# Performance work log

Hardware: AMD Instinct MI355X
Metric: run time of the kernel (lower is better)

## Reference

```python
import jax, jax.numpy as jnp
import numpy as np

N_HEAD = 16
ROPE_THETA = 10000.0


def _rope_cache(T, dim, theta=ROPE_THETA):
    # inv_freq over even indices, as in RotaryEmbedding
    inv_freq = 1.0 / (theta ** (jnp.arange(0, dim, 2, dtype=jnp.float32) / dim))
    freqs = jnp.arange(T, dtype=jnp.float32)[:, None] * inv_freq[None, :]  # [T, dim//2]
    return jnp.cos(freqs), jnp.sin(freqs)


def _apply_rope(x, cos, sin):
    # x: [B, H, T, D]; cos/sin: [T, D//2] broadcast over B,H
    x1 = x[..., ::2]
    x2 = x[..., 1::2]
    # even slots: x1*cos - x2*sin ; odd slots: x2*cos + x1*sin (interleaved rotate-pairs)
    r1 = x1 * cos - x2 * sin
    r2 = x2 * cos + x1 * sin
    return jnp.stack([r1, r2], axis=-1).reshape(x.shape)


def setup_inputs() -> dict:
    key = jax.random.key(0)
    k1, k2, k3 = jax.random.split(key, 3)
    B, T, C = 4, 2048, 1024
    x = jax.random.normal(k1, (B, T, C), dtype=jnp.float32)
    W_qkv = jax.random.normal(k2, (C, 3 * C), dtype=jnp.float32) * (C ** -0.5)
    W_out = jax.random.normal(k3, (C, C), dtype=jnp.float32) * (C ** -0.5)
    return {"x": x, "W_qkv": W_qkv, "W_out": W_out}


def reference(x, W_qkv, W_out):
    B, T, C = x.shape
    H = N_HEAD
    D = C // H
    # fused QKV projection -> [3, B, H, T, D]
    qkv = (x @ W_qkv).reshape(B, T, 3, H, D).transpose(2, 0, 3, 1, 4)
    q, k, v = qkv[0], qkv[1], qkv[2]
    cos, sin = _rope_cache(T, D)
    q = _apply_rope(q, cos, sin)
    k = _apply_rope(k, cos, sin)
    scale = 1.0 / jnp.sqrt(jnp.float32(D))
    scores = jnp.einsum('bhqd,bhkd->bhqk', q, k) * scale  # [B,H,T,T]
    causal_mask = jnp.tril(jnp.ones((T, T), dtype=bool))
    scores = jnp.where(causal_mask, scores, -jnp.inf)
    attn = jax.nn.softmax(scores, axis=-1)
    out = jnp.einsum('bhqk,bhkd->bhqd', attn, v)  # [B,H,T,D]
    out = out.transpose(0, 2, 1, 3).reshape(B, T, C)
    return out @ W_out
```

## Files before the change

kernel.cpp:

```cpp
#include <hip/hip_runtime.h>
#include <math.h>

#define BATCH 4
#define SEQ   2048
#define CDIM  1024
#define NHEAD 16
#define HDIM  64
#define QKVN  3072
#define QSCALE 0.1803368801111244f

typedef float f32x4 __attribute__((ext_vector_type(4)));
typedef short bf16x8 __attribute__((ext_vector_type(8)));
typedef short bf16x4 __attribute__((ext_vector_type(4)));

static __device__ __forceinline__ unsigned short f2bf(float f) {
    unsigned int u = __float_as_uint(f);
    u += 0x7FFF + ((u >> 16) & 1);
    return (unsigned short)(u >> 16);
}
static __device__ __forceinline__ float bf2f(unsigned short u) {
    return __uint_as_float(((unsigned int)u) << 16);
}
static __device__ __forceinline__ bf16x8 lds_read8(const unsigned short* p) {
    bf16x4 lo = *(const bf16x4*)p;
    bf16x4 hi = *(const bf16x4*)(p + 4);
    return __builtin_shufflevector(lo, hi, 0, 1, 2, 3, 4, 5, 6, 7);
}

__global__ __launch_bounds__(256) void convert_bf16(const float* __restrict__ src,
                                                    unsigned short* __restrict__ dst,
                                                    int n4) {
    int i = blockIdx.x * 256 + threadIdx.x;
    if (i >= n4) return;
    float4 v = ((const float4*)src)[i];
    ushort4 o;
    o.x = f2bf(v.x); o.y = f2bf(v.y); o.z = f2bf(v.z); o.w = f2bf(v.w);
    ((ushort4*)dst)[i] = o;
}

__global__ __launch_bounds__(256) void transpose_bf16(const float* __restrict__ W,
                                                      unsigned short* __restrict__ Wt,
                                                      int K, int N) {
    __shared__ unsigned short tile[64][65];
    const int tid = threadIdx.x;
    const int n0 = blockIdx.x * 64;
    const int k0 = blockIdx.y * 64;
    const int r = tid >> 4;
    const int c4 = (tid & 15) << 2;
    #pragma unroll
    for (int ii = 0; ii < 4; ii++) {
        int row = r + 16 * ii;
        float4 v = *(const float4*)&W[(size_t)(k0 + row) * N + n0 + c4];
        tile[c4 + 0][row] = f2bf(v.x);
        tile[c4 + 1][row] = f2bf(v.y);
        tile[c4 + 2][row] = f2bf(v.z);
        tile[c4 + 3][row] = f2bf(v.w);
    }
    __syncthreads();
    #pragma unroll
    for (int ii = 0; ii < 4; ii++) {
        int row = r + 16 * ii;
        ushort4 o;
        o.x = tile[row][c4 + 0];
        o.y = tile[row][c4 + 1];
        o.z = tile[row][c4 + 2];
        o.w = tile[row][c4 + 3];
        *(ushort4*)&Wt[(size_t)(n0 + row) * K + k0 + c4] = o;
    }
}

#define GLDS(gp, lp) __builtin_amdgcn_global_load_lds(                       \
    (const __attribute__((address_space(1))) unsigned int*)(gp),             \
    (__attribute__((address_space(3))) unsigned int*)(lp), 16, 0, 0)

template <typename OUT>
__global__ __launch_bounds__(256) void gemm_bt_bf16(
    const unsigned short* __restrict__ A,
    const unsigned short* __restrict__ Bt,
    OUT* __restrict__ C, int M, int N, int K) {
    __shared__ unsigned short As[128 * 32];
    __shared__ unsigned short Bs[128 * 32];

    const int tid = threadIdx.x;
    const int wave = tid >> 6;
    const int lane = tid & 63;
    const int bm = blockIdx.y * 128;
    const int bn = blockIdx.x * 128;
    const int wm = (wave >> 1) * 64;
    const int wn = (wave & 1) * 64;

    const int srow = tid >> 2;
    const int scol = (tid & 3) << 3;
    const unsigned short* Ag0 = A + (size_t)(bm + srow) * K + scol;
    const unsigned short* Ag1 = A + (size_t)(bm + 64 + srow) * K + scol;
    const unsigned short* Bg0 = Bt + (size_t)(bn + srow) * K + scol;
    const unsigned short* Bg1 = Bt + (size_t)(bn + 64 + srow) * K + scol;
    char* AsW = (char*)As + wave * 1024;
    char* BsW = (char*)Bs + wave * 1024;

    const int fm = lane & 15;
    const int fq = (lane >> 4) << 3;

    f32x4 acc[4][4];
    #pragma unroll
    for (int i = 0; i < 4; i++)
        #pragma unroll
        for (int j = 0; j < 4; j++)
            acc[i][j] = (f32x4){0.f, 0.f, 0.f, 0.f};

    for (int k0 = 0; k0 < K; k0 += 32) {
        GLDS(Ag0 + k0, AsW);
        GLDS(Ag1 + k0, AsW + 4096);
        GLDS(Bg0 + k0, BsW);
        GLDS(Bg1 + k0, BsW + 4096);
        __syncthreads();

        bf16x8 af[4], bfr[4];
        #pragma unroll
        for (int i = 0; i < 4; i++)
            af[i] = *(const bf16x8*)&As[(wm + i * 16 + fm) * 32 + fq];
        #pragma unroll
        for (int j = 0; j < 4; j++)
            bfr[j] = *(const bf16x8*)&Bs[(wn + j * 16 + fm) * 32 + fq];
        #pragma unroll
        for (int i = 0; i < 4; i++)
            #pragma unroll
            for (int j = 0; j < 4; j++)
                acc[i][j] = __builtin_amdgcn_mfma_f32_16x16x32_bf16(
                    af[i], bfr[j], acc[i][j], 0, 0, 0);
        __syncthreads();
    }

    const int er = (lane >> 4) * 4;
    #pragma unroll
    for (int i = 0; i < 4; i++) {
        #pragma unroll
        for (int j = 0; j < 4; j++) {
            #pragma unroll
            for (int r = 0; r < 4; r++) {
                size_t off = (size_t)(bm + wm + i * 16 + er + r) * N + bn + wn + j * 16 + fm;
                if constexpr (sizeof(OUT) == 2)
                    C[off] = f2bf(acc[i][j][r]);
                else
                    C[off] = acc[i][j][r];
            }
        }
    }
}

__global__ __launch_bounds__(256) void rope_qk(const unsigned short* __restrict__ qkvb,
                                               unsigned short* __restrict__ Qg,
                                               unsigned short* __restrict__ Kg) {
    const int i = blockIdx.x * 256 + threadIdx.x;
    const int c4 = (i & 15) << 2;
    const int h = (i >> 4) & 15;
    const int s = (i >> 8) & 1;
    const int t = (i >> 9) & 2047;
    const int b = i >> 20;

    ushort4 v = *(const ushort4*)&qkvb[(((size_t)(b * SEQ + t) * 3 + s) * CDIM) + h * HDIM + c4];
    float x0 = bf2f(v.x), x1 = bf2f(v.y), x2 = bf2f(v.z), x3 = bf2f(v.w);
    const float invf0 = powf(10000.0f, -((float)c4) / 64.0f);
    const float invf1 = powf(10000.0f, -((float)(c4 + 2)) / 64.0f);
    float s0, c0, s1, c1;
    __sincosf((float)t * invf0, &s0, &c0);
    __sincosf((float)t * invf1, &s1, &c1);
    const float sc = s == 0 ? QSCALE : 1.0f;
    ushort4 o;
    o.x = f2bf((x0 * c0 - x1 * s0) * sc);
    o.y = f2bf((x1 * c0 + x0 * s0) * sc);
    o.z = f2bf((x2 * c1 - x3 * s1) * sc);
    o.w = f2bf((x3 * c1 + x2 * s1) * sc);
    unsigned short* dst = (s == 0) ? Qg : Kg;
    *(ushort4*)&dst[((size_t)(b * NHEAD + h) * SEQ + t) * HDIM + c4] = o;
}

__global__ __launch_bounds__(256) void transpose_v(const unsigned short* __restrict__ qkvb,
                                                   unsigned short* __restrict__ Vtg) {
    __shared__ unsigned short tile[64 * 68];
    const int tid = threadIdx.x;
    const int tt = blockIdx.x;
    const int bh = blockIdx.y;
    const int b = bh >> 4, h = bh & 15;
    const int r = tid >> 4;
    const int c4 = (tid & 15) << 2;
    #pragma unroll
    for (int ii = 0; ii < 4; ii++) {
        int row = r + 16 * ii;
        ushort4 v = *(const ushort4*)&qkvb[(((size_t)(b * SEQ + tt * 64 + row) * 3 + 2) * CDIM) + h * HDIM + c4];
        *(ushort4*)&tile[row * 68 + c4] = v;
    }
    __syncthreads();
    #pragma unroll
    for (int ii = 0; ii < 4; ii++) {
        int d = r + 16 * ii;
        ushort4 o;
        o.x = tile[(c4 + 0) * 68 + d];
        o.y = tile[(c4 + 1) * 68 + d];
        o.z = tile[(c4 + 2) * 68 + d];
        o.w = tile[(c4 + 3) * 68 + d];
        *(ushort4*)&Vtg[((size_t)bh * HDIM + d) * SEQ + tt * 64 + c4] = o;
    }
}

__global__ __launch_bounds__(256, 3) void flash_attn_mfma(
    const unsigned short* __restrict__ Qg,
    const unsigned short* __restrict__ Kg,
    const unsigned short* __restrict__ Vtg,
    unsigned short* __restrict__ att) {
    __shared__ unsigned short Ks[64 * 68];
    __shared__ unsigned short Vt[64 * 68];
    __shared__ unsigned short Ps[128 * 68];

    const int tid = threadIdx.x;
    const int wave = tid >> 6;
    const int lane = tid & 63;
    const int fm = lane & 15;
    const int quad = lane >> 4;
    const int fq = quad << 3;
    const int wq = wave * 32;
    const int bh = blockIdx.x & 63;
    const int qt = 15 - (blockIdx.x >> 6);
    const int b = bh >> 4, h = bh & 15;

    const int r_ld = tid >> 4;
    const int c4 = (tid & 15) << 2;

    bf16x8 aq[2][2];
    #pragma unroll
    for (int i = 0; i < 2; i++)
        #pragma unroll
        for (int ks = 0; ks < 2; ks++)
            aq[i][ks] = *(const bf16x8*)&Qg[((size_t)bh * SEQ + qt * 128 + wq + i * 16 + fm) * HDIM + ks * 32 + fq];

    bf16x8 bones;
    #pragma unroll
    for (int z = 0; z < 8; z++) bones[z] = (short)0x3F80;

    f32x4 O[2][4], lsum[2];
    #pragma unroll
    for (int i = 0; i < 2; i++) {
        lsum[i] = (f32x4){0.f, 0.f, 0.f, 0.f};
        #pragma unroll
        for (int dt = 0; dt < 4; dt++) O[i][dt] = (f32x4){0.f, 0.f, 0.f, 0.f};
    }

    const int jtop = 2 * qt + 1;
    for (int j = 0; j <= jtop; j++) {
        #pragma unroll
        for (int ii = 0; ii < 4; ii++) {
            const int row = r_ld + 16 * ii;
            *(ushort4*)&Ks[row * 68 + c4] =
                *(const ushort4*)&Kg[((size_t)bh * SEQ + j * 64 + row) * HDIM + c4];
            *(ushort4*)&Vt[row * 68 + c4] =
                *(const ushort4*)&Vtg[((size_t)bh * HDIM + row) * SEQ + j * 64 + c4];
        }
        __syncthreads();

        const bool active = (j * 64) <= (qt * 128 + wq + 31);
        if (active) {
            f32x4 sa[2][4];
            #pragma unroll
            for (int i = 0; i < 2; i++)
                #pragma unroll
                for (int jj = 0; jj < 4; jj++)
                    sa[i][jj] = (f32x4){0.f, 0.f, 0.f, 0.f};
            #pragma unroll
            for (int ks = 0; ks < 2; ks++) {
                #pragma unroll
                for (int jj = 0; jj < 4; jj++) {
                    bf16x8 bk = lds_read8(&Ks[(jj * 16 + fm) * 68 + ks * 32 + fq]);
                    sa[0][jj] = __builtin_amdgcn_mfma_f32_16x16x32_bf16(aq[0][ks], bk, sa[0][jj], 0, 0, 0);
                    sa[1][jj] = __builtin_amdgcn_mfma_f32_16x16x32_bf16(aq[1][ks], bk, sa[1][jj], 0, 0, 0);
                }
            }

            if (j * 64 + 63 > qt * 128 + wq) {
                const int kb = j * 64 + fm;
                #pragma unroll
                for (int i = 0; i < 2; i++) {
                    const int rb = qt * 128 + wq + i * 16 + quad * 4;
                    #pragma unroll
                    for (int jj = 0; jj < 4; jj++)
                        #pragma unroll
                        for (int r = 0; r < 4; r++)
                            if (kb + jj * 16 > rb + r) sa[i][jj][r] = -INFINITY;
                }
            }

            #pragma unroll
            for (int i = 0; i < 2; i++) {
                const int prow = (wq + i * 16 + quad * 4) * 68 + fm;
                #pragma unroll
                for (int jj = 0; jj < 4; jj++)
                    #pragma unroll
                    for (int r = 0; r < 4; r++)
                        Ps[prow + r * 68 + jj * 16] = f2bf(exp2f(sa[i][jj][r]));
            }

            #pragma unroll
            for (int ks = 0; ks < 2; ks++) {
                bf16x8 ap0 = lds_read8(&Ps[(wq + fm) * 68 + ks * 32 + fq]);
                bf16x8 ap1 = lds_read8(&Ps[(wq + 16 + fm) * 68 + ks * 32 + fq]);
                lsum[0] = __builtin_amdgcn_mfma_f32_16x16x32_bf16(ap0, bones, lsum[0], 0, 0, 0);
                lsum[1] = __builtin_amdgcn_mfma_f32_16x16x32_bf16(ap1, bones, lsum[1], 0, 0, 0);
                #pragma unroll
                for (int dt = 0; dt < 4; dt++) {
                    bf16x8 bv = lds_read8(&Vt[(dt * 16 + fm) * 68 + ks * 32 + fq]);
                    O[0][dt] = __builtin_amdgcn_mfma_f32_16x16x32_bf16(ap0, bv, O[0][dt], 0, 0, 0);
                    O[1][dt] = __builtin_amdgcn_mfma_f32_16x16x32_bf16(ap1, bv, O[1][dt], 0, 0, 0);
                }
            }
        }
        __syncthreads();
    }

    #pragma unroll
    for (int i = 0; i < 2; i++) {
        #pragma unroll
        for (int r = 0; r < 4; r++) {
            const float inv_l = 1.0f / lsum[i][r];
            const int row = qt * 128 + wq + i * 16 + quad * 4 + r;
            #pragma unroll
            for (int dt = 0; dt < 4; dt++)
                att[(size_t)(b * SEQ + row) * CDIM + h * HDIM + dt * 16 + fm] =
                    f2bf(O[i][dt][r] * inv_l);
        }
    }
}

extern "C" void kernel_launch(void* const* d_in, const int* in_sizes, int n_in,
                              void* d_out, int out_size, void* d_ws, size_t ws_size,
                              hipStream_t stream) {
    const float* x     = (const float*)d_in[0];
    const float* W_qkv = (const float*)d_in[1];
    const float* W_out = (const float*)d_in[2];
    float* out = (float*)d_out;

    const int M = BATCH * SEQ;

    unsigned short* qkvb = (unsigned short*)d_ws;
    unsigned short* xb   = qkvb + (size_t)M * QKVN;
    unsigned short* wqb  = xb + (size_t)M * CDIM;
    unsigned short* wob  = wqb + (size_t)CDIM * QKVN;
    unsigned short* attb = wob + (size_t)CDIM * CDIM;
    unsigned short* Qg   = attb + (size_t)M * CDIM;
    unsigned short* Kg   = Qg + (size_t)M * CDIM;
    unsigned short* Vtg  = Kg + (size_t)M * CDIM;

    convert_bf16<<<(M * CDIM / 4 + 255) / 256, 256, 0, stream>>>(x, xb, M * CDIM / 4);
    transpose_bf16<<<dim3(QKVN / 64, CDIM / 64), 256, 0, stream>>>(W_qkv, wqb, CDIM, QKVN);
    transpose_bf16<<<dim3(CDIM / 64, CDIM / 64), 256, 0, stream>>>(W_out, wob, CDIM, CDIM);

    gemm_bt_bf16<unsigned short><<<dim3(QKVN / 128, M / 128), 256, 0, stream>>>(
        xb, wqb, qkvb, M, QKVN, CDIM);

    rope_qk<<<(BATCH * SEQ * 2 * NHEAD * 16) / 256, 256, 0, stream>>>(qkvb, Qg, Kg);
    transpose_v<<<dim3(SEQ / 64, BATCH * NHEAD), 256, 0, stream>>>(qkvb, Vtg);

    flash_attn_mfma<<<BATCH * NHEAD * (SEQ / 128), 256, 0, stream>>>(Qg, Kg, Vtg, attb);

    gemm_bt_bf16<float><<<dim3(CDIM / 128, M / 128), 256, 0, stream>>>(
        attb, wob, out, M, CDIM, CDIM);
}
```

Before: 311.6 us.

## Swizzle GEMM LDS layout, raise attention occupancy, pack bf16 conversion

The GEMM now XOR-swizzles the K-chunk column used for global-to-LDS staging and applies the matching swizzle on the fragment reads, to cut LDS bank conflicts. The flash attention kernel's launch bounds go from 3 to 4 blocks per SIMD, trading register budget for occupancy, which risks spills. The softmax probability conversion uses the packed bf16x2 round-to-nearest intrinsic instead of the manual per-element rounding. These are three independent tweaks.

```diff
diff --git a/kernel.cpp b/kernel.cpp
--- a/kernel.cpp
+++ b/kernel.cpp
@@ -1,4 +1,5 @@
 #include <hip/hip_runtime.h>
+#include <hip/hip_bf16.h>
 #include <math.h>
 
 #define BATCH 4
@@ -20,6 +21,10 @@
 }
 static __device__ __forceinline__ float bf2f(unsigned short u) {
     return __uint_as_float(((unsigned int)u) << 16);
+}
+static __device__ __forceinline__ unsigned int pk2bf(float lo, float hi) {
+    __hip_bfloat162 h = __float22bfloat162_rn(make_float2(lo, hi));
+    return *(unsigned int*)&h;
 }
 static __device__ __forceinline__ bf16x8 lds_read8(const unsigned short* p) {
     bf16x4 lo = *(const bf16x4*)p;
@@ -90,7 +95,7 @@
     const int wn = (wave & 1) * 64;
 
     const int srow = tid >> 2;
-    const int scol = (tid & 3) << 3;
+    const int scol = (((tid & 3) ^ ((tid >> 3) & 3)) << 3);
     const unsigned short* Ag0 = A + (size_t)(bm + srow) * K + scol;
     const unsigned short* Ag1 = A + (size_t)(bm + 64 + srow) * K + scol;
     const unsigned short* Bg0 = Bt + (size_t)(bn + srow) * K + scol;
@@ -99,7 +104,8 @@
     char* BsW = (char*)Bs + wave * 1024;
 
     const int fm = lane & 15;
-    const int fq = (lane >> 4) << 3;
+    const int quad = lane >> 4;
+    const int ck = (quad ^ ((fm >> 1) & 3)) << 3;
 
     f32x4 acc[4][4];
     #pragma unroll
@@ -118,10 +124,10 @@
         bf16x8 af[4], bfr[4];
         #pragma unroll
         for (int i = 0; i < 4; i++)
-            af[i] = *(const bf16x8*)&As[(wm + i * 16 + fm) * 32 + fq];
+            af[i] = *(const bf16x8*)&As[(wm + i * 16 + fm) * 32 + ck];
         #pragma unroll
         for (int j = 0; j < 4; j++)
-            bfr[j] = *(const bf16x8*)&Bs[(wn + j * 16 + fm) * 32 + fq];
+            bfr[j] = *(const bf16x8*)&Bs[(wn + j * 16 + fm) * 32 + ck];
         #pragma unroll
         for (int i = 0; i < 4; i++)
             #pragma unroll
@@ -131,7 +137,7 @@
         __syncthreads();
     }
 
-    const int er = (lane >> 4) * 4;
+    const int er = quad * 4;
     #pragma unroll
     for (int i = 0; i < 4; i++) {
         #pragma unroll
@@ -203,7 +209,7 @@
     }
 }
 
-__global__ __launch_bounds__(256, 3) void flash_attn_mfma(
+__global__ __launch_bounds__(256, 4) void flash_attn_mfma(
     const unsigned short* __restrict__ Qg,
     const unsigned short* __restrict__ Kg,
     const unsigned short* __restrict__ Vtg,
@@ -292,10 +298,18 @@
             for (int i = 0; i < 2; i++) {
                 const int prow = (wq + i * 16 + quad * 4) * 68 + fm;
                 #pragma unroll
-                for (int jj = 0; jj < 4; jj++)
-                    #pragma unroll
-                    for (int r = 0; r < 4; r++)
-                        Ps[prow + r * 68 + jj * 16] = f2bf(exp2f(sa[i][jj][r]));
+                for (int jj = 0; jj < 4; jj++) {
+                    const float e0 = exp2f(sa[i][jj][0]);
+                    const float e1 = exp2f(sa[i][jj][1]);
+                    const float e2 = exp2f(sa[i][jj][2]);
+                    const float e3 = exp2f(sa[i][jj][3]);
+                    const unsigned int p01 = pk2bf(e0, e1);
+                    const unsigned int p23 = pk2bf(e2, e3);
+                    Ps[prow + 0 * 68 + jj * 16] = (unsigned short)p01;
+                    Ps[prow + 1 * 68 + jj * 16] = (unsigned short)(p01 >> 16);
+                    Ps[prow + 2 * 68 + jj * 16] = (unsigned short)p23;
+                    Ps[prow + 3 * 68 + jj * 16] = (unsigned short)(p23 >> 16);
+                }
             }
 
             #pragma unroll
```

New measurement: 307.9 us. No clear change (-1.2%).
